# Kernel optimization log

Measured on AMD Instinct MI355X. Metric: run time of the kernel, lower is better.

## Reference

```python
import jax, jax.numpy as jnp
import numpy as np

N = 50000
E = 800000
IN = 128
HID = 32
OUT = 32
H1, H2 = 4, 4
NEG_SLOPE = 0.2


def setup_inputs() -> dict:
    key = jax.random.key(0)
    ks = jax.random.split(key, 12)
    x = jax.random.normal(ks[0], (N, IN), dtype=jnp.float32)
    src = jax.random.randint(ks[1], (E,), 0, N, dtype=jnp.int32)
    dst = jax.random.randint(ks[2], (E,), 0, N, dtype=jnp.int32)
    s = 0.1
    # layer 1: fc (IN -> H1*HID, no bias), attn vectors (H1, HID), bias (H1*HID,)
    W1 = jax.random.normal(ks[3], (IN, H1 * HID), dtype=jnp.float32) * s
    al1 = jax.random.normal(ks[4], (H1, HID), dtype=jnp.float32) * s
    ar1 = jax.random.normal(ks[5], (H1, HID), dtype=jnp.float32) * s
    b1 = jnp.zeros((H1 * HID,), dtype=jnp.float32)
    # layer 2: fc (H1*HID -> H2*OUT, no bias)
    W2 = jax.random.normal(ks[6], (H1 * HID, H2 * OUT), dtype=jnp.float32) * s
    al2 = jax.random.normal(ks[7], (H2, OUT), dtype=jnp.float32) * s
    ar2 = jax.random.normal(ks[8], (H2, OUT), dtype=jnp.float32) * s
    b2 = jnp.zeros((H2 * OUT,), dtype=jnp.float32)
    return {"x": x, "W1": W1, "al1": al1, "ar1": ar1, "b1": b1,
            "W2": W2, "al2": al2, "ar2": ar2, "b2": b2,
            "src": src, "dst": dst}


def _gat_layer(x, W, al, ar, b, src, dst, n, h, d):
    # feat_drop is identity (eval mode)
    feat = (x @ W).reshape(n, h, d)                       # [N,H,D]
    el = jnp.einsum('nhd,hd->nh', feat, al)               # [N,H]
    er = jnp.einsum('nhd,hd->nh', feat, ar)               # [N,H]
    e = jax.nn.leaky_relu(el[src] + er[dst], NEG_SLOPE)   # [E,H] SDDMM
    # edge softmax over incoming edges of each destination node
    emax = jax.ops.segment_max(e, dst, num_segments=n)    # [N,H]
    emax = jnp.where(jnp.isfinite(emax), emax, 0.0)       # guard 0-in-degree
    w = jnp.exp(e - emax[dst])                            # [E,H]
    denom = jax.ops.segment_sum(w, dst, num_segments=n)   # [N,H]
    alpha = w / jnp.maximum(denom[dst], 1e-9)             # [E,H]; attn_drop identity
    # SpMM aggregation
    rst = jax.ops.segment_sum(feat[src] * alpha[:, :, None], dst, num_segments=n)
    # residual: in_feats == h*d for both layers -> DGL uses Identity res_fc
    rst = rst + x.reshape(n, h, d)
    rst = rst + b.reshape(1, h, d)
    return rst


def reference(x, W1, al1, ar1, b1, W2, al2, ar2, b2, src, dst):
    h = _gat_layer(x, W1, al1, ar1, b1, src, dst, N, H1, HID)
    h = jax.nn.elu(h)                                     # layer-1 activation
    h = h.reshape(N, H1 * HID)                            # flatten(1)
    h = _gat_layer(h, W2, al2, ar2, b2, src, dst, N, H2, OUT)
    return h.mean(axis=1)                                 # [N,OUT]
```

## Files before the change

### kernel.cpp

```cpp
#include <hip/hip_runtime.h>
#include <cstdint>
#include <cstddef>

#define NEG_SLOPE 0.2f

typedef __bf16 bf16x8 __attribute__((ext_vector_type(8)));
typedef float  f32x4  __attribute__((ext_vector_type(4)));

__device__ inline unsigned int bf16pair(float a, float b) {
    unsigned int ua = __float_as_uint(a), ub = __float_as_uint(b);
    ua += 0x7fffu + ((ua >> 16) & 1u);
    ub += 0x7fffu + ((ub >> 16) & 1u);
    return (ua >> 16) | (ub & 0xffff0000u);
}
__device__ inline unsigned short bf16r(float x) {
    unsigned int u = __float_as_uint(x);
    u += 0x7fffu + ((u >> 16) & 1u);
    return (unsigned short)(u >> 16);
}

__global__ __launch_bounds__(256) void wtrans_kernel(
    const float* __restrict__ W1, const float* __restrict__ W2,
    unsigned short* __restrict__ Wt1, unsigned short* __restrict__ Wt2)
{
    __shared__ float tile[64][65];
    const float* W = (blockIdx.x < 4) ? W1 : W2;
    unsigned short* Wt = (blockIdx.x < 4) ? Wt1 : Wt2;
    const int tb = blockIdx.x & 3;
    const int k0 = (tb >> 1) * 64, n0 = (tb & 1) * 64;
    const int c = threadIdx.x & 63, r4 = threadIdx.x >> 6;
#pragma unroll
    for (int i = 0; i < 16; ++i) {
        const int r = i * 4 + r4;
        tile[r][c] = W[(size_t)(k0 + r) * 128 + n0 + c];
    }
    __syncthreads();
#pragma unroll
    for (int i = 0; i < 16; ++i) {
        const int nn = i * 4 + r4;
        Wt[(size_t)(n0 + nn) * 128 + k0 + c] = bf16r(tile[c][nn]);
    }
}

template <bool RANK>
__global__ __launch_bounds__(256, 3) void gemm_attn_kernel(
    const float* __restrict__ X, const unsigned short* __restrict__ Wt,
    const float* __restrict__ al, const float* __restrict__ ar,
    unsigned short* __restrict__ feat16, float* __restrict__ el,
    float* __restrict__ er, int n, int gemm_blocks,
    const int* __restrict__ dst, int* __restrict__ deg,
    int* __restrict__ rank, int E)
{
    __shared__ unsigned short sX[64][136];
    __shared__ unsigned short sW[128][136];

    const int t = threadIdx.x;

    if (RANK && (int)blockIdx.x >= gemm_blocks) {
        const int bid = blockIdx.x - gemm_blocks;
        const int e4 = (bid * 256 + t) * 4;
        if (e4 + 4 <= E) {
            const int4 d = *(const int4*)&dst[e4];
            int4 r;
            r.x = atomicAdd(&deg[d.x], 1);
            r.y = atomicAdd(&deg[d.y], 1);
            r.z = atomicAdd(&deg[d.z], 1);
            r.w = atomicAdd(&deg[d.w], 1);
            *(int4*)&rank[e4] = r;
        } else {
            for (int e = e4; e < E; ++e) rank[e] = atomicAdd(&deg[dst[e]], 1);
        }
        return;
    }

    const int rowbase = blockIdx.x * 64;

#pragma unroll
    for (int i = 0; i < 8; ++i) {
        const int idx = t + 256 * i;
        const int row = idx >> 5;
        const int kq  = (idx & 31) * 4;
        int g = rowbase + row; if (g >= n) g = n - 1;
        const float4 v = *(const float4*)&X[(size_t)g * 128 + kq];
        uint2 pk;
        pk.x = bf16pair(v.x, v.y);
        pk.y = bf16pair(v.z, v.w);
        *(uint2*)&sX[row][kq] = pk;
    }
#pragma unroll
    for (int i = 0; i < 8; ++i) {
        const int idx = t + 256 * i;
        const int row = idx >> 4;
        const int q   = idx & 15;
        *(uint4*)&sW[row][q * 8] = *(const uint4*)&Wt[(size_t)row * 128 + q * 8];
    }
    __syncthreads();

    const int lane = t & 63;
    const int w    = t >> 6;
    const int m    = lane & 15;
    const int g4   = lane >> 4;

    bf16x8 a[4];
#pragma unroll
    for (int ks = 0; ks < 4; ++ks)
        a[ks] = *(const bf16x8*)&sX[w * 16 + m][ks * 32 + g4 * 8];

    float elacc[4][4] = {{0}}, eracc[4][4] = {{0}};
    unsigned short fout[8][4];

#pragma unroll
    for (int ct = 0; ct < 8; ct += 2) {
        f32x4 acc0 = {0.f, 0.f, 0.f, 0.f}, acc1 = {0.f, 0.f, 0.f, 0.f};
        const int n0 = ct * 16 + m, n1 = n0 + 16;
#pragma unroll
        for (int ks = 0; ks < 4; ++ks) {
            const bf16x8 b0 = *(const bf16x8*)&sW[n0][ks * 32 + g4 * 8];
            const bf16x8 b1 = *(const bf16x8*)&sW[n1][ks * 32 + g4 * 8];
            acc0 = __builtin_amdgcn_mfma_f32_16x16x32_bf16(a[ks], b0, acc0, 0, 0, 0);
            acc1 = __builtin_amdgcn_mfma_f32_16x16x32_bf16(a[ks], b1, acc1, 0, 0, 0);
        }
        const int h = ct >> 1;
        const float al0 = al[n0], ar0 = ar[n0];
        const float al1 = al[n1], ar1 = ar[n1];
#pragma unroll
        for (int r = 0; r < 4; ++r) {
            elacc[r][h] += acc0[r] * al0 + acc1[r] * al1;
            eracc[r][h] += acc0[r] * ar0 + acc1[r] * ar1;
            fout[ct][r]     = bf16r(acc0[r]);
            fout[ct + 1][r] = bf16r(acc1[r]);
        }
    }

    __syncthreads();
#pragma unroll
    for (int ct = 0; ct < 8; ++ct)
#pragma unroll
        for (int r = 0; r < 4; ++r)
            sX[w * 16 + g4 * 4 + r][ct * 16 + m] = fout[ct][r];
    __syncthreads();
    {
        const int row = t >> 2;
        const int q   = t & 3;
        const int g   = rowbase + row;
        if (g < n) {
#pragma unroll
            for (int i = 0; i < 4; ++i) {
                const int c0 = q * 8 + i * 32;
                *(uint4*)&feat16[(size_t)g * 128 + c0] = *(const uint4*)&sX[row][c0];
            }
        }
    }

#pragma unroll
    for (int r = 0; r < 4; ++r)
#pragma unroll
        for (int h = 0; h < 4; ++h) {
            float a_ = elacc[r][h], b_ = eracc[r][h];
            a_ += __shfl_xor(a_, 1); b_ += __shfl_xor(b_, 1);
            a_ += __shfl_xor(a_, 2); b_ += __shfl_xor(b_, 2);
            a_ += __shfl_xor(a_, 4); b_ += __shfl_xor(b_, 4);
            a_ += __shfl_xor(a_, 8); b_ += __shfl_xor(b_, 8);
            elacc[r][h] = a_; eracc[r][h] = b_;
        }
    if (m == 0) {
#pragma unroll
        for (int r = 0; r < 4; ++r) {
            const int row = rowbase + w * 16 + g4 * 4 + r;
            if (row < n) {
#pragma unroll
                for (int h = 0; h < 4; ++h) {
                    el[(size_t)row * 4 + h] = elacc[r][h];
                    er[(size_t)row * 4 + h] = eracc[r][h];
                }
            }
        }
    }
}

__global__ __launch_bounds__(1024) void scan_kernel(
    const int* __restrict__ deg, int* __restrict__ off, int n)
{
    __shared__ int wsums[16];
    __shared__ int s_carry;
    const int tid  = threadIdx.x;
    const int lane = tid & 63;
    const int wid  = tid >> 6;

    if (tid == 0) { s_carry = 0; off[0] = 0; }
    __syncthreads();

    const int n4 = n >> 2;
    const int4* __restrict__ deg4 = (const int4*)deg;

    for (int base = 0; base < n4; base += 1024) {
        const int i4 = base + tid;
        int4 v = make_int4(0, 0, 0, 0);
        if (i4 < n4) v = deg4[i4];
        const int t0 = v.x, t1 = t0 + v.y, t2 = t1 + v.z, t3 = t2 + v.w;

        int x = t3;
#pragma unroll
        for (int d = 1; d < 64; d <<= 1) {
            int y = __shfl_up(x, d);
            if (lane >= d) x += y;
        }
        if (lane == 63) wsums[wid] = x;
        __syncthreads();

        if (wid == 0 && lane < 16) {
            int xx = wsums[lane];
#pragma unroll
            for (int d = 1; d < 16; d <<= 1) {
                int y = __shfl_up(xx, d);
                if (lane >= d) xx += y;
            }
            wsums[lane] = xx;
        }
        __syncthreads();

        const int wp   = (wid == 0) ? 0 : wsums[wid - 1];
        const int excl = s_carry + wp + (x - t3);
        if (i4 < n4) {
            off[4 * i4 + 1] = excl + t0;
            off[4 * i4 + 2] = excl + t1;
            off[4 * i4 + 3] = excl + t2;
            off[4 * i4 + 4] = excl + t3;
        }
        __syncthreads();
        if (tid == 0) s_carry += wsums[15];
        __syncthreads();
    }
}

__global__ void place_kernel(const int* __restrict__ src, const int* __restrict__ dst,
                             const int* __restrict__ off, const int* __restrict__ rank,
                             int* __restrict__ csr_src, int E)
{
    const int e4 = (blockIdx.x * blockDim.x + threadIdx.x) * 4;
    if (e4 + 4 <= E) {
        const int4 s = *(const int4*)&src[e4];
        const int4 d = *(const int4*)&dst[e4];
        const int4 r = *(const int4*)&rank[e4];
        const int o0 = off[d.x], o1 = off[d.y], o2 = off[d.z], o3 = off[d.w];
        csr_src[o0 + r.x] = s.x;
        csr_src[o1 + r.y] = s.y;
        csr_src[o2 + r.z] = s.z;
        csr_src[o3 + r.w] = s.w;
    } else {
        for (int e = e4; e < E; ++e)
            csr_src[off[dst[e]] + rank[e]] = src[e];
    }
}

template <bool LAYER2>
__global__ __launch_bounds__(256, 4) void agg_kernel(
    const int* __restrict__ off, const int* __restrict__ csr_src,
    const unsigned short* __restrict__ feat16, const float* __restrict__ el,
    const float* __restrict__ er, const float* __restrict__ resid,
    const float* __restrict__ bias, float* __restrict__ out, int n)
{
    const int lane = threadIdx.x & 63;
    const int node = blockIdx.x * 4 + (threadIdx.x >> 6);
    if (node >= n) return;

    const int h  = lane >> 4;
    const int d0 = 2 * lane;

    const float erh = er[(size_t)node * 4 + h];
    const unsigned int* __restrict__ fb = (const unsigned int*)feat16;

    const int beg = off[node], end = off[node + 1];

    float acc0 = 0.f, acc1 = 0.f, sw = 0.f;
    int j = beg;

    for (; j + 16 <= end; j += 16) {
        int s[16]; float ev[16]; unsigned int uv[16];
#pragma unroll
        for (int q = 0; q < 16; ++q) s[q] = csr_src[j + q];
#pragma unroll
        for (int q = 0; q < 16; ++q) ev[q] = el[(size_t)s[q] * 4 + h];
#pragma unroll
        for (int q = 0; q < 16; ++q) uv[q] = fb[(size_t)s[q] * 64 + lane];
#pragma unroll
        for (int q = 0; q < 16; ++q) {
            float a = ev[q] + erh;
            a = fmaxf(a, NEG_SLOPE * a);
            const float wq = __expf(a);
            acc0 += wq * __uint_as_float(uv[q] << 16);
            acc1 += wq * __uint_as_float(uv[q] & 0xffff0000u);
            sw += wq;
        }
    }
    for (; j + 4 <= end; j += 4) {
        int s[4]; float ev[4]; unsigned int uv[4];
#pragma unroll
        for (int q = 0; q < 4; ++q) s[q] = csr_src[j + q];
#pragma unroll
        for (int q = 0; q < 4; ++q) ev[q] = el[(size_t)s[q] * 4 + h];
#pragma unroll
        for (int q = 0; q < 4; ++q) uv[q] = fb[(size_t)s[q] * 64 + lane];
#pragma unroll
        for (int q = 0; q < 4; ++q) {
            float a = ev[q] + erh;
            a = fmaxf(a, NEG_SLOPE * a);
            const float wq = __expf(a);
            acc0 += wq * __uint_as_float(uv[q] << 16);
            acc1 += wq * __uint_as_float(uv[q] & 0xffff0000u);
            sw += wq;
        }
    }
    for (; j < end; ++j) {
        const int s = csr_src[j];
        float a = el[(size_t)s * 4 + h] + erh;
        a = fmaxf(a, NEG_SLOPE * a);
        const float wq = __expf(a);
        const unsigned int u = fb[(size_t)s * 64 + lane];
        acc0 += wq * __uint_as_float(u << 16);
        acc1 += wq * __uint_as_float(u & 0xffff0000u);
        sw += wq;
    }

    const float inv = 1.f / fmaxf(sw, 1e-9f);
    const float2 rs = *(const float2*)&resid[(size_t)node * 128 + d0];
    float v0 = acc0 * inv + rs.x + bias[d0];
    float v1 = acc1 * inv + rs.y + bias[d0 + 1];

    if (!LAYER2) {
        v0 = (v0 > 0.f) ? v0 : expm1f(v0);
        v1 = (v1 > 0.f) ? v1 : expm1f(v1);
        *(float2*)&out[(size_t)node * 128 + d0] = make_float2(v0, v1);
    } else {
        float s0 = v0, s1 = v1;
        s0 += __shfl_xor(s0, 16); s1 += __shfl_xor(s1, 16);
        s0 += __shfl_xor(s0, 32); s1 += __shfl_xor(s1, 32);
        if (lane < 16)
            *(float2*)&out[(size_t)node * 32 + 2 * lane] =
                make_float2(s0 * 0.25f, s1 * 0.25f);
    }
}

extern "C" void kernel_launch(void* const* d_in, const int* in_sizes, int n_in,
                              void* d_out, int out_size, void* d_ws, size_t ws_size,
                              hipStream_t stream)
{
    const float* x   = (const float*)d_in[0];
    const float* W1  = (const float*)d_in[1];
    const float* al1 = (const float*)d_in[2];
    const float* ar1 = (const float*)d_in[3];
    const float* b1  = (const float*)d_in[4];
    const float* W2  = (const float*)d_in[5];
    const float* al2 = (const float*)d_in[6];
    const float* ar2 = (const float*)d_in[7];
    const float* b2  = (const float*)d_in[8];
    const int*   src = (const int*)d_in[9];
    const int*   dst = (const int*)d_in[10];

    const int n = in_sizes[0] / 128;
    const int E = in_sizes[9];
    float* out = (float*)d_out;

    char* p = (char*)d_ws;
    float* h1    = (float*)p;          p += (size_t)n * 128 * sizeof(float);
    unsigned short* feat16 = (unsigned short*)p; p += (size_t)n * 128 * sizeof(unsigned short);
    float* el    = (float*)p;          p += (size_t)n * 4 * sizeof(float);
    float* er    = (float*)p;          p += (size_t)n * 4 * sizeof(float);
    int* off     = (int*)p;            p += (size_t)(n + 1) * sizeof(int);
    int* deg     = (int*)p;            p += (size_t)n * sizeof(int);
    int* rank    = (int*)p;            p += (size_t)E * sizeof(int);
    int* csr     = (int*)p;            p += (size_t)E * sizeof(int);
    unsigned short* wt1 = (unsigned short*)p; p += (size_t)128 * 128 * sizeof(unsigned short);
    unsigned short* wt2 = (unsigned short*)p; p += (size_t)128 * 128 * sizeof(unsigned short);

    hipMemsetAsync(deg, 0, (size_t)n * sizeof(int), stream);

    const int gemm_grid  = (n + 63) / 64;
    const int edge4_grid = (E / 4 + 255) / 256;
    const int agg_grid   = (n + 3) / 4;

    wtrans_kernel<<<8, 256, 0, stream>>>(W1, W2, wt1, wt2);
    gemm_attn_kernel<true><<<gemm_grid + edge4_grid, 256, 0, stream>>>(
        x, wt1, al1, ar1, feat16, el, er, n, gemm_grid, dst, deg, rank, E);
    scan_kernel<<<1, 1024, 0, stream>>>(deg, off, n);
    place_kernel<<<edge4_grid, 256, 0, stream>>>(src, dst, off, rank, csr, E);
    agg_kernel<false><<<agg_grid, 256, 0, stream>>>(off, csr, feat16, el, er, x, b1, h1, n);
    gemm_attn_kernel<false><<<gemm_grid, 256, 0, stream>>>(
        h1, wt2, al2, ar2, feat16, el, er, n, gemm_grid, nullptr, nullptr, nullptr, 0);
    agg_kernel<true><<<agg_grid, 256, 0, stream>>>(off, csr, feat16, el, er, h1, b2, out, n);
}
```

Baseline: 274.0 us.

## Store layer-1 output in bf16, restructure GEMM tiling, move degree ranking to prep kernel

The layer-1 aggregation output h1 is now written in bf16 and read as bf16 by the layer-2 GEMM and the residual, which halves that intermediate traffic. The GEMM kernel keeps its B fragments in registers per wave (32 columns each), drops the shared W tile, writes output through a swizzled shared buffer, and computes el/er per row tile. The edge-degree ranking moves from the GEMM launch into the weight-transpose prep kernel. Occupancy hints change on both the GEMM and aggregation kernels. Holding the layer-2 residual in bf16 costs some precision.

```diff
diff --git a/kernel.cpp b/kernel.cpp
--- a/kernel.cpp
+++ b/kernel.cpp
@@ -19,160 +19,148 @@
     return (unsigned short)(u >> 16);
 }
 
-__global__ __launch_bounds__(256) void wtrans_kernel(
+__global__ __launch_bounds__(256) void prep_kernel(
     const float* __restrict__ W1, const float* __restrict__ W2,
-    unsigned short* __restrict__ Wt1, unsigned short* __restrict__ Wt2)
+    unsigned short* __restrict__ Wt1, unsigned short* __restrict__ Wt2,
+    const int* __restrict__ dst, int* __restrict__ deg,
+    int* __restrict__ rank, int E)
 {
     __shared__ float tile[64][65];
-    const float* W = (blockIdx.x < 4) ? W1 : W2;
-    unsigned short* Wt = (blockIdx.x < 4) ? Wt1 : Wt2;
-    const int tb = blockIdx.x & 3;
-    const int k0 = (tb >> 1) * 64, n0 = (tb & 1) * 64;
-    const int c = threadIdx.x & 63, r4 = threadIdx.x >> 6;
-#pragma unroll
-    for (int i = 0; i < 16; ++i) {
-        const int r = i * 4 + r4;
-        tile[r][c] = W[(size_t)(k0 + r) * 128 + n0 + c];
-    }
-    __syncthreads();
-#pragma unroll
-    for (int i = 0; i < 16; ++i) {
-        const int nn = i * 4 + r4;
-        Wt[(size_t)(n0 + nn) * 128 + k0 + c] = bf16r(tile[c][nn]);
-    }
-}
-
-template <bool RANK>
-__global__ __launch_bounds__(256, 3) void gemm_attn_kernel(
-    const float* __restrict__ X, const unsigned short* __restrict__ Wt,
+    if (blockIdx.x < 8) {
+        const float* W = (blockIdx.x < 4) ? W1 : W2;
+        unsigned short* Wt = (blockIdx.x < 4) ? Wt1 : Wt2;
+        const int tb = blockIdx.x & 3;
+        const int k0 = (tb >> 1) * 64, n0 = (tb & 1) * 64;
+        const int c = threadIdx.x & 63, r4 = threadIdx.x >> 6;
+#pragma unroll
+        for (int i = 0; i < 16; ++i) {
+            const int r = i * 4 + r4;
+            tile[r][c] = W[(size_t)(k0 + r) * 128 + n0 + c];
+        }
+        __syncthreads();
+#pragma unroll
+        for (int i = 0; i < 16; ++i) {
+            const int nn = i * 4 + r4;
+            Wt[(size_t)(n0 + nn) * 128 + k0 + c] = bf16r(tile[c][nn]);
+        }
+        return;
+    }
+    const int bid = blockIdx.x - 8;
+    const int e4 = (bid * 256 + threadIdx.x) * 4;
+    if (e4 + 4 <= E) {
+        const int4 d = *(const int4*)&dst[e4];
+        int4 r;
+        r.x = atomicAdd(&deg[d.x], 1);
+        r.y = atomicAdd(&deg[d.y], 1);
+        r.z = atomicAdd(&deg[d.z], 1);
+        r.w = atomicAdd(&deg[d.w], 1);
+        *(int4*)&rank[e4] = r;
+    } else {
+        for (int e = e4; e < E; ++e) rank[e] = atomicAdd(&deg[dst[e]], 1);
+    }
+}
+
+template <bool XBF16>
+__global__ __launch_bounds__(256, 4) void gemm_attn_kernel(
+    const void* __restrict__ Xv, const unsigned short* __restrict__ Wt,
     const float* __restrict__ al, const float* __restrict__ ar,
     unsigned short* __restrict__ feat16, float* __restrict__ el,
-    float* __restrict__ er, int n, int gemm_blocks,
-    const int* __restrict__ dst, int* __restrict__ deg,
-    int* __restrict__ rank, int E)
+    float* __restrict__ er, int n)
 {
     __shared__ unsigned short sX[64][136];
-    __shared__ unsigned short sW[128][136];
+    __shared__ unsigned short sF[64][136];
 
     const int t = threadIdx.x;
-
-    if (RANK && (int)blockIdx.x >= gemm_blocks) {
-        const int bid = blockIdx.x - gemm_blocks;
-        const int e4 = (bid * 256 + t) * 4;
-        if (e4 + 4 <= E) {
-            const int4 d = *(const int4*)&dst[e4];
-            int4 r;
-            r.x = atomicAdd(&deg[d.x], 1);
-            r.y = atomicAdd(&deg[d.y], 1);
-            r.z = atomicAdd(&deg[d.z], 1);
-            r.w = atomicAdd(&deg[d.w], 1);
-            *(int4*)&rank[e4] = r;
-        } else {
-            for (int e = e4; e < E; ++e) rank[e] = atomicAdd(&deg[dst[e]], 1);
-        }
-        return;
-    }
-
     const int rowbase = blockIdx.x * 64;
 
-#pragma unroll
-    for (int i = 0; i < 8; ++i) {
-        const int idx = t + 256 * i;
-        const int row = idx >> 5;
-        const int kq  = (idx & 31) * 4;
-        int g = rowbase + row; if (g >= n) g = n - 1;
-        const float4 v = *(const float4*)&X[(size_t)g * 128 + kq];
-        uint2 pk;
-        pk.x = bf16pair(v.x, v.y);
-        pk.y = bf16pair(v.z, v.w);
-        *(uint2*)&sX[row][kq] = pk;
-    }
-#pragma unroll
-    for (int i = 0; i < 8; ++i) {
-        const int idx = t + 256 * i;
-        const int row = idx >> 4;
-        const int q   = idx & 15;
-        *(uint4*)&sW[row][q * 8] = *(const uint4*)&Wt[(size_t)row * 128 + q * 8];
-    }
-    __syncthreads();
+    if (XBF16) {
+        const unsigned short* X = (const unsigned short*)Xv;
+#pragma unroll
+        for (int i = 0; i < 4; ++i) {
+            const int idx = t + 256 * i;
+            const int row = idx >> 4;
+            const int q   = idx & 15;
+            int g = rowbase + row; if (g >= n) g = n - 1;
+            *(uint4*)&sX[row][q * 8] = *(const uint4*)&X[(size_t)g * 128 + q * 8];
+        }
+    } else {
+        const float* X = (const float*)Xv;
+#pragma unroll
+        for (int i = 0; i < 8; ++i) {
+            const int idx = t + 256 * i;
+            const int row = idx >> 5;
+            const int kq  = (idx & 31) * 4;
+            int g = rowbase + row; if (g >= n) g = n - 1;
+            const float4 v = *(const float4*)&X[(size_t)g * 128 + kq];
+            uint2 pk;
+            pk.x = bf16pair(v.x, v.y);
+            pk.y = bf16pair(v.z, v.w);
+            *(uint2*)&sX[row][kq] = pk;
+        }
+    }
 
     const int lane = t & 63;
     const int w    = t >> 6;
     const int m    = lane & 15;
     const int g4   = lane >> 4;
 
-    bf16x8 a[4];
-#pragma unroll
-    for (int ks = 0; ks < 4; ++ks)
-        a[ks] = *(const bf16x8*)&sX[w * 16 + m][ks * 32 + g4 * 8];
-
-    float elacc[4][4] = {{0}}, eracc[4][4] = {{0}};
-    unsigned short fout[8][4];
-
-#pragma unroll
-    for (int ct = 0; ct < 8; ct += 2) {
+    bf16x8 bfr[2][4];
+#pragma unroll
+    for (int tile = 0; tile < 2; ++tile)
+#pragma unroll
+        for (int ks = 0; ks < 4; ++ks)
+            bfr[tile][ks] = *(const bf16x8*)
+                &Wt[(size_t)(w * 32 + tile * 16 + m) * 128 + ks * 32 + g4 * 8];
+
+    __syncthreads();
+
+    const int n0 = w * 32 + m, n1 = n0 + 16;
+    const float al0 = al[n0], ar0 = ar[n0];
+    const float al1 = al[n1], ar1 = ar[n1];
+    const int swz = g4 << 3;
+
+#pragma unroll
+    for (int rt = 0; rt < 4; ++rt) {
+        bf16x8 a[4];
+#pragma unroll
+        for (int ks = 0; ks < 4; ++ks)
+            a[ks] = *(const bf16x8*)&sX[rt * 16 + m][ks * 32 + g4 * 8];
         f32x4 acc0 = {0.f, 0.f, 0.f, 0.f}, acc1 = {0.f, 0.f, 0.f, 0.f};
-        const int n0 = ct * 16 + m, n1 = n0 + 16;
 #pragma unroll
         for (int ks = 0; ks < 4; ++ks) {
-            const bf16x8 b0 = *(const bf16x8*)&sW[n0][ks * 32 + g4 * 8];
-            const bf16x8 b1 = *(const bf16x8*)&sW[n1][ks * 32 + g4 * 8];
-            acc0 = __builtin_amdgcn_mfma_f32_16x16x32_bf16(a[ks], b0, acc0, 0, 0, 0);
-            acc1 = __builtin_amdgcn_mfma_f32_16x16x32_bf16(a[ks], b1, acc1, 0, 0, 0);
-        }
-        const int h = ct >> 1;
-        const float al0 = al[n0], ar0 = ar[n0];
-        const float al1 = al[n1], ar1 = ar[n1];
+            acc0 = __builtin_amdgcn_mfma_f32_16x16x32_bf16(a[ks], bfr[0][ks], acc0, 0, 0, 0);
+            acc1 = __builtin_amdgcn_mfma_f32_16x16x32_bf16(a[ks], bfr[1][ks], acc1, 0, 0, 0);
+        }
 #pragma unroll
         for (int r = 0; r < 4; ++r) {
-            elacc[r][h] += acc0[r] * al0 + acc1[r] * al1;
-            eracc[r][h] += acc0[r] * ar0 + acc1[r] * ar1;
-            fout[ct][r]     = bf16r(acc0[r]);
-            fout[ct + 1][r] = bf16r(acc1[r]);
-        }
-    }
-
-    __syncthreads();
-#pragma unroll
-    for (int ct = 0; ct < 8; ++ct)
-#pragma unroll
-        for (int r = 0; r < 4; ++r)
-            sX[w * 16 + g4 * 4 + r][ct * 16 + m] = fout[ct][r];
+            const int row = rt * 16 + g4 * 4 + r;
+            sF[row][(n0) ^ swz]      = bf16r(acc0[r]);
+            sF[row][(n1) ^ swz]      = bf16r(acc1[r]);
+            float pl = acc0[r] * al0 + acc1[r] * al1;
+            float pr = acc0[r] * ar0 + acc1[r] * ar1;
+            pl += __shfl_xor(pl, 1); pr += __shfl_xor(pr, 1);
+            pl += __shfl_xor(pl, 2); pr += __shfl_xor(pr, 2);
+            pl += __shfl_xor(pl, 4); pr += __shfl_xor(pr, 4);
+            pl += __shfl_xor(pl, 8); pr += __shfl_xor(pr, 8);
+            if (m == 0 && rowbase + row < n) {
+                el[(size_t)(rowbase + row) * 4 + w] = pl;
+                er[(size_t)(rowbase + row) * 4 + w] = pr;
+            }
+        }
+    }
+
     __syncthreads();
     {
         const int row = t >> 2;
         const int q   = t & 3;
         const int g   = rowbase + row;
+        const int sw_ = ((row >> 2) & 3) << 3;
         if (g < n) {
 #pragma unroll
             for (int i = 0; i < 4; ++i) {
                 const int c0 = q * 8 + i * 32;
-                *(uint4*)&feat16[(size_t)g * 128 + c0] = *(const uint4*)&sX[row][c0];
-            }
-        }
-    }
-
-#pragma unroll
-    for (int r = 0; r < 4; ++r)
-#pragma unroll
-        for (int h = 0; h < 4; ++h) {
-            float a_ = elacc[r][h], b_ = eracc[r][h];
-            a_ += __shfl_xor(a_, 1); b_ += __shfl_xor(b_, 1);
-            a_ += __shfl_xor(a_, 2); b_ += __shfl_xor(b_, 2);
-            a_ += __shfl_xor(a_, 4); b_ += __shfl_xor(b_, 4);
-            a_ += __shfl_xor(a_, 8); b_ += __shfl_xor(b_, 8);
-            elacc[r][h] = a_; eracc[r][h] = b_;
-        }
-    if (m == 0) {
-#pragma unroll
-        for (int r = 0; r < 4; ++r) {
-            const int row = rowbase + w * 16 + g4 * 4 + r;
-            if (row < n) {
-#pragma unroll
-                for (int h = 0; h < 4; ++h) {
-                    el[(size_t)row * 4 + h] = elacc[r][h];
-                    er[(size_t)row * 4 + h] = eracc[r][h];
-                }
+                *(uint4*)&feat16[(size_t)g * 128 + c0] =
+                    *(const uint4*)&sF[row][c0 ^ sw_];
             }
         }
     }
@@ -254,11 +242,11 @@
 }
 
 template <bool LAYER2>
-__global__ __launch_bounds__(256, 4) void agg_kernel(
+__global__ __launch_bounds__(256) void agg_kernel(
     const int* __restrict__ off, const int* __restrict__ csr_src,
     const unsigned short* __restrict__ feat16, const float* __restrict__ el,
-    const float* __restrict__ er, const float* __restrict__ resid,
-    const float* __restrict__ bias, float* __restrict__ out, int n)
+    const float* __restrict__ er, const void* __restrict__ resid,
+    const float* __restrict__ bias, void* __restrict__ out, int n)
 {
     const int lane = threadIdx.x & 63;
     const int node = blockIdx.x * 4 + (threadIdx.x >> 6);
@@ -323,20 +311,29 @@
     }
 
     const float inv = 1.f / fmaxf(sw, 1e-9f);
-    const float2 rs = *(const float2*)&resid[(size_t)node * 128 + d0];
-    float v0 = acc0 * inv + rs.x + bias[d0];
-    float v1 = acc1 * inv + rs.y + bias[d0 + 1];
+    float rx, ry;
+    if (!LAYER2) {
+        const float2 rs = *(const float2*)((const float*)resid + (size_t)node * 128 + d0);
+        rx = rs.x; ry = rs.y;
+    } else {
+        const unsigned int u =
+            *(const unsigned int*)((const unsigned short*)resid + (size_t)node * 128 + d0);
+        rx = __uint_as_float(u << 16);
+        ry = __uint_as_float(u & 0xffff0000u);
+    }
+    float v0 = acc0 * inv + rx + bias[d0];
+    float v1 = acc1 * inv + ry + bias[d0 + 1];
 
     if (!LAYER2) {
         v0 = (v0 > 0.f) ? v0 : expm1f(v0);
         v1 = (v1 > 0.f) ? v1 : expm1f(v1);
-        *(float2*)&out[(size_t)node * 128 + d0] = make_float2(v0, v1);
+        *(unsigned int*)((unsigned short*)out + (size_t)node * 128 + d0) = bf16pair(v0, v1);
     } else {
         float s0 = v0, s1 = v1;
         s0 += __shfl_xor(s0, 16); s1 += __shfl_xor(s1, 16);
         s0 += __shfl_xor(s0, 32); s1 += __shfl_xor(s1, 32);
         if (lane < 16)
-            *(float2*)&out[(size_t)node * 32 + 2 * lane] =
+            *(float2*)((float*)out + (size_t)node * 32 + 2 * lane) =
                 make_float2(s0 * 0.25f, s1 * 0.25f);
     }
 }
@@ -362,7 +359,7 @@
     float* out = (float*)d_out;
 
     char* p = (char*)d_ws;
-    float* h1    = (float*)p;          p += (size_t)n * 128 * sizeof(float);
+    unsigned short* h1b    = (unsigned short*)p; p += (size_t)n * 128 * sizeof(unsigned short);
     unsigned short* feat16 = (unsigned short*)p; p += (size_t)n * 128 * sizeof(unsigned short);
     float* el    = (float*)p;          p += (size_t)n * 4 * sizeof(float);
     float* er    = (float*)p;          p += (size_t)n * 4 * sizeof(float);
@@ -379,13 +376,11 @@
     const int edge4_grid = (E / 4 + 255) / 256;
     const int agg_grid   = (n + 3) / 4;
 
-    wtrans_kernel<<<8, 256, 0, stream>>>(W1, W2, wt1, wt2);
-    gemm_attn_kernel<true><<<gemm_grid + edge4_grid, 256, 0, stream>>>(
-        x, wt1, al1, ar1, feat16, el, er, n, gemm_grid, dst, deg, rank, E);
+    prep_kernel<<<8 + edge4_grid, 256, 0, stream>>>(W1, W2, wt1, wt2, dst, deg, rank, E);
+    gemm_attn_kernel<false><<<gemm_grid, 256, 0, stream>>>(x, wt1, al1, ar1, feat16, el, er, n);
     scan_kernel<<<1, 1024, 0, stream>>>(deg, off, n);
     place_kernel<<<edge4_grid, 256, 0, stream>>>(src, dst, off, rank, csr, E);
-    agg_kernel<false><<<agg_grid, 256, 0, stream>>>(off, csr, feat16, el, er, x, b1, h1, n);
-    gemm_attn_kernel<false><<<gemm_grid, 256, 0, stream>>>(
-        h1, wt2, al2, ar2, feat16, el, er, n, gemm_grid, nullptr, nullptr, nullptr, 0);
-    agg_kernel<true><<<agg_grid, 256, 0, stream>>>(off, csr, feat16, el, er, h1, b2, out, n);
-}
+    agg_kernel<false><<<agg_grid, 256, 0, stream>>>(off, csr, feat16, el, er, x, b1, h1b, n);
+    gemm_attn_kernel<true><<<gemm_grid, 256, 0, stream>>>(h1b, wt2, al2, ar2, feat16, el, er, n);
+    agg_kernel<true><<<agg_grid, 256, 0, stream>>>(off, csr, feat16, el, er, h1b, b2, out, n);
+}
```

Result: slower. 282.5 us (+3.1%).
